# Kernel optimization log

Measured on AMD Instinct MI355X. Metric: run time of the kernel, lower is better.

Reference implementation:

```python
import jax, jax.numpy as jnp
import numpy as np

B_, L, DM = 2, 1024, 1024
D_STATE, D_CONV, EXPAND = 16, 4, 2
DI = EXPAND * DM          # 2048 inner dim
DTR = DM // 16            # 64 dt rank


def setup_inputs() -> dict:
    key = jax.random.key(0)
    ks = jax.random.split(key, 16)
    g = lambda k, shp, s: jax.random.normal(k, shp, jnp.float32) * s
    inp = {
        "x": g(ks[0], (B_, L, DM), 1.0),
        "ln_g": jnp.ones((DM,), jnp.float32),
        "ln_b": jnp.zeros((DM,), jnp.float32),
        "in_proj_w": g(ks[1], (2 * DI, DM), (2.0 / (DM + 2 * DI)) ** 0.5),
        "conv_w": g(ks[2], (DI, 1, D_CONV), (2.0 / D_CONV) ** 0.5),
        "conv_b": jnp.zeros((DI,), jnp.float32),
        "dtin_w": g(ks[3], (DTR, DI), (2.0 / (DI + DTR)) ** 0.5),
        "dtin_b": jnp.zeros((DTR,), jnp.float32),
        "dt_w": g(ks[4], (DI, DTR), DTR ** -0.5),
        "dt_b": jnp.log(jnp.expm1(jax.random.uniform(ks[5], (DI,), jnp.float32, 1e-3, 0.1))),  # inverse-softplus of dt in [dt_min, dt_max]
        "B_w": g(ks[6], (D_STATE, DI), DI ** -0.5),
        "C_w": g(ks[7], (D_STATE, DI), DI ** -0.5),
        "A_log": jnp.log(jnp.broadcast_to(jnp.arange(1, D_STATE + 1, dtype=jnp.float32), (DI, D_STATE))),
        "D": jnp.ones((DI,), jnp.float32),
        "out_w": g(ks[8], (DM, DI), (2.0 / (DM + DI)) ** 0.5),
    }
    return inp


def _layernorm(x, g, b, eps=1e-5):
    mu = jnp.mean(x, -1, keepdims=True)
    var = jnp.mean(jnp.square(x - mu), -1, keepdims=True)
    return (x - mu) * jax.lax.rsqrt(var + eps) * g + b


def _selective_scan(u, dt, Bm, Cm, A, Dp):
    # u,dt: (b,l,di); Bm,Cm: (b,l,n); A: (di,n)
    def step(h, inp):
        dt_t, B_t, C_t, u_t = inp  # (b,di),(b,n),(b,n),(b,di)
        dA = jnp.exp(dt_t[..., None] * A)                       # (b,di,n)
        h = h * dA + (dt_t * u_t)[..., None] * B_t[:, None, :]   # (b,di,n)
        y = jnp.einsum("bdn,bn->bd", h, C_t)
        return h, y

    tm = lambda a: jnp.swapaxes(a, 0, 1)  # time-major
    h0 = jnp.zeros((u.shape[0], u.shape[2], A.shape[1]), u.dtype)
    _, ys = jax.lax.scan(step, h0, (tm(dt), tm(Bm), tm(Cm), tm(u)))
    return jnp.swapaxes(ys, 0, 1) + u * Dp  # (b,l,di)


def reference(x, ln_g, ln_b, in_proj_w, conv_w, conv_b, dtin_w, dtin_b,
              dt_w, dt_b, B_w, C_w, A_log, D, out_w):
    residual = x
    xn = _layernorm(x, ln_g, ln_b)
    xz = xn @ in_proj_w.T                       # (b,l,2*di)
    x_proj, z = jnp.split(xz, 2, axis=-1)
    # causal depthwise conv1d (left pad d_conv-1, truncate to seq_len)
    xp = jnp.pad(x_proj, ((0, 0), (D_CONV - 1, 0), (0, 0)))
    x_conv = conv_b
    for k in range(D_CONV):
        x_conv = x_conv + conv_w[:, 0, k] * xp[:, k:k + L, :]
    x_conv = jax.nn.silu(x_conv)
    dt_in = x_conv @ dtin_w.T + dtin_b          # (b,l,dtr)
    dt = jax.nn.softplus(dt_in @ dt_w.T + dt_b) # (b,l,di)
    Bm = x_conv @ B_w.T                         # (b,l,n)
    Cm = x_conv @ C_w.T
    A = -jnp.exp(A_log)                         # (di,n)
    y = _selective_scan(x_conv, dt, Bm, Cm, A, D)
    y = y * jax.nn.silu(z)
    return y @ out_w.T + residual
```

## Files before the change

### kernel.cpp

```cpp
#include <hip/hip_runtime.h>
#include <hip/hip_bf16.h>
#include <cstdint>

#define BL    2
#define LSEQ  1024
#define DMOD  1024
#define DIN   2048
#define NST   16
#define DTRK  64
#define MR    (BL*LSEQ)

#define CCH 32
#define TCH 32
#define KSPLIT 8

typedef __bf16 bf16x8 __attribute__((ext_vector_type(8)));
typedef float  f32x4  __attribute__((ext_vector_type(4)));

#if __has_builtin(__builtin_amdgcn_exp2f)
#define EXP2F(x) __builtin_amdgcn_exp2f(x)
#else
#define EXP2F(x) exp2f(x)
#endif
#define LOG2E 1.4426950408889634f

__device__ __forceinline__ void glds16(const void* g, const void* l) {
    __builtin_amdgcn_global_load_lds(
        (__attribute__((address_space(1))) void*)(uintptr_t)(g),
        (__attribute__((address_space(3))) void*)(uint32_t)(uintptr_t)(l),
        16, 0, 0);
}

template <int MODE, int TM, int TN, int BK>
__global__ __launch_bounds__(256, 3) void gemm_bt(
    const __hip_bfloat16* __restrict__ A, int lda,
    const __hip_bfloat16* __restrict__ Bw, int ldb,
    int M, int N, int Ksl,
    void* __restrict__ e0, void* __restrict__ e1,
    const float* __restrict__ bias)
{
    constexpr int WM = TM / 2, WN = TN / 2;
    constexpr int MT = WM / 16, NT = WN / 16;
    constexpr int C8 = BK / 8;
    constexpr int RPP = 256 / C8;
    constexpr int PA = TM / RPP, PB = TN / RPP;
    __shared__ __align__(16) __hip_bfloat16 sA[2][TM * BK];
    __shared__ __align__(16) __hip_bfloat16 sB[2][TN * BK];

    auto SW = [](int row) { return (BK == 32) ? ((row >> 1) & 3) : (row & 7); };

    int bx = blockIdx.x, by = blockIdx.y;
    if ((gridDim.y & 7) == 0) {
        const int bid = blockIdx.x + gridDim.x * blockIdx.y;
        const int xcd = bid & 7, s = bid >> 3;
        bx = s % gridDim.x;
        by = (s / gridDim.x) * 8 + xcd;
    }
    const int m0 = by * TM;
    const int n0 = bx * TN;
    const int k0 = blockIdx.z * Ksl;
    const int tid = threadIdx.x;
    const int w = tid >> 6, lane = tid & 63;
    const int wm = (w >> 1) * WM, wn = (w & 1) * WN;
    const int lrow = lane & 15, lq = lane >> 4;

    const int r0 = tid / C8;
    const int q = ((tid % C8) - SW(r0)) & (C8 - 1);
    const __hip_bfloat16* pa[PA];
    const __hip_bfloat16* pb[PB];
#pragma unroll
    for (int p = 0; p < PA; p++) pa[p] = A + (size_t)(m0 + r0 + RPP * p) * lda + k0 + q * 8;
#pragma unroll
    for (int p = 0; p < PB; p++) pb[p] = Bw + (size_t)(n0 + r0 + RPP * p) * ldb + k0 + q * 8;

    f32x4 acc[MT][NT];
#pragma unroll
    for (int i = 0; i < MT; i++)
#pragma unroll
        for (int j = 0; j < NT; j++) { acc[i][j][0]=0.f; acc[i][j][1]=0.f; acc[i][j][2]=0.f; acc[i][j][3]=0.f; }

    const int nk = Ksl / BK;
#pragma unroll
    for (int p = 0; p < PA; p++) glds16(pa[p], &sA[0][(tid + 256 * p) * 8]);
#pragma unroll
    for (int p = 0; p < PB; p++) glds16(pb[p], &sB[0][(tid + 256 * p) * 8]);

    for (int kb = 0; kb < nk; ++kb) {
        const int cur = kb & 1, nxt = cur ^ 1;
        __syncthreads();
        if (kb + 1 < nk) {
#pragma unroll
            for (int p = 0; p < PA; p++) { pa[p] += BK; glds16(pa[p], &sA[nxt][(tid + 256 * p) * 8]); }
#pragma unroll
            for (int p = 0; p < PB; p++) { pb[p] += BK; glds16(pb[p], &sB[nxt][(tid + 256 * p) * 8]); }
        }
#pragma unroll
        for (int s = 0; s < BK / 32; s++) {
            bf16x8 af[MT], bb[NT];
#pragma unroll
            for (int mt = 0; mt < MT; mt++) {
                const int row = wm + mt * 16 + lrow;
                const int pc = ((s * 4 + lq) + SW(row)) & (C8 - 1);
                af[mt] = *(const bf16x8*)&sA[cur][row * BK + pc * 8];
            }
#pragma unroll
            for (int nt = 0; nt < NT; nt++) {
                const int row = wn + nt * 16 + lrow;
                const int pc = ((s * 4 + lq) + SW(row)) & (C8 - 1);
                bb[nt] = *(const bf16x8*)&sB[cur][row * BK + pc * 8];
            }
#pragma unroll
            for (int mt = 0; mt < MT; mt++)
#pragma unroll
                for (int nt = 0; nt < NT; nt++)
                    acc[mt][nt] = __builtin_amdgcn_mfma_f32_16x16x32_bf16(af[mt], bb[nt], acc[mt][nt], 0, 0, 0);
        }
    }

#pragma unroll
    for (int mt = 0; mt < MT; mt++) {
#pragma unroll
        for (int nt = 0; nt < NT; nt++) {
            const int gn = n0 + wn + nt * 16 + lrow;
            if (gn >= N) continue;
            const int gmb = m0 + wm + mt * 16 + lq * 4;
#pragma unroll
            for (int r = 0; r < 4; r++) {
                const int gm = gmb + r;
                const float v = acc[mt][nt][r];
                if (MODE == 0) {
                    if (gn < DIN) ((__hip_bfloat16*)e0)[(size_t)gm * DIN + gn] = __float2bfloat16(v);
                    else {
                        const float s = v / (1.f + __expf(-v));
                        ((__hip_bfloat16*)e1)[(size_t)gm * DIN + (gn - DIN)] = __float2bfloat16(s);
                    }
                } else if (MODE == 1) {
                    ((float*)e0)[((size_t)blockIdx.z * M + gm) * 96 + gn] = v;
                } else if (MODE == 2) {
                    const float xx = v + bias[gn];
                    const float sp = (xx > 20.f) ? xx : log1pf(__expf(xx));
                    ((__hip_bfloat16*)e0)[(size_t)gm * N + gn] = __float2bfloat16(sp);
                } else {
                    atomicAdd((float*)e0 + (size_t)gm * N + gn, v);
                }
            }
        }
    }
}

__global__ void ep1_kernel(const float* __restrict__ part, const float* __restrict__ dtin_b,
                           __hip_bfloat16* __restrict__ dtinb, float* __restrict__ Bmf,
                           float* __restrict__ Cmf) {
    const int i = blockIdx.x * 256 + threadIdx.x;
    if (i >= MR * 96) return;
    const int m = i / 96, n = i - m * 96;
    float s = 0.f;
#pragma unroll
    for (int z = 0; z < KSPLIT; z++) s += part[((size_t)z * MR + m) * 96 + n];
    if (n < 64)      dtinb[(size_t)m * 64 + n] = __float2bfloat16(s + dtin_b[n]);
    else if (n < 80) Bmf[(size_t)m * NST + (n - 64)] = s;
    else             Cmf[(size_t)m * NST + (n - 80)] = s;
}

#define NCVT 1654784
#define NCPY 524288
__global__ void prep_kernel(const float* __restrict__ x, const float* __restrict__ ln_g,
                            const float* __restrict__ ln_b,
                            const float* __restrict__ w_in, const float* __restrict__ dtin_w,
                            const float* __restrict__ B_w, const float* __restrict__ C_w,
                            const float* __restrict__ dt_w, const float* __restrict__ out_w,
                            __hip_bfloat16* __restrict__ w1b, __hip_bfloat16* __restrict__ wpb,
                            __hip_bfloat16* __restrict__ dtwb, __hip_bfloat16* __restrict__ owb,
                            __hip_bfloat16* __restrict__ xn, float* __restrict__ out)
{
    const int b = blockIdx.x;
    const int tid = threadIdx.x;
    if (b < MR) {
        const float4 v = ((const float4*)(x + (size_t)b * DMOD))[tid];
        float s  = v.x + v.y + v.z + v.w;
        float sq = v.x * v.x + v.y * v.y + v.z * v.z + v.w * v.w;
#pragma unroll
        for (int off = 32; off >= 1; off >>= 1) {
            s  += __shfl_down(s, off, 64);
            sq += __shfl_down(sq, off, 64);
        }
        __shared__ float red[8];
        const int w = tid >> 6, lane = tid & 63;
        if (lane == 0) { red[w] = s; red[4 + w] = sq; }
        __syncthreads();
        s  = red[0] + red[1] + red[2] + red[3];
        sq = red[4] + red[5] + red[6] + red[7];
        const float mean = s * (1.f / DMOD);
        const float rstd = rsqrtf(sq * (1.f / DMOD) - mean * mean + 1e-5f);
        const int col = tid * 4;
        const float vv[4] = {v.x, v.y, v.z, v.w};
#pragma unroll
        for (int i = 0; i < 4; i++)
            xn[(size_t)b * DMOD + col + i] =
                __float2bfloat16((vv[i] - mean) * rstd * ln_g[col + i] + ln_b[col + i]);
        return;
    }
    const int nb = gridDim.x - MR;
    for (int v4 = (b - MR) * 256 + tid; v4 < NCVT + NCPY; v4 += nb * 256) {
        if (v4 >= NCVT) {
            ((float4*)out)[v4 - NCVT] = ((const float4*)x)[v4 - NCVT];
            continue;
        }
        const int i = v4 * 4;
        const float* s; __hip_bfloat16* dk;
        if      (i < 4194304) { s = w_in   + i;             dk = w1b  + i; }
        else if (i < 4325376) { s = dtin_w + (i - 4194304); dk = wpb  + (i - 4194304); }
        else if (i < 4358144) { s = B_w    + (i - 4325376); dk = wpb  + 131072 + (i - 4325376); }
        else if (i < 4390912) { s = C_w    + (i - 4358144); dk = wpb  + 163840 + (i - 4358144); }
        else if (i < 4521984) { s = dt_w   + (i - 4390912); dk = dtwb + (i - 4390912); }
        else                  { s = out_w  + (i - 4521984); dk = owb  + (i - 4521984); }
        const float4 f = *(const float4*)s;
        ushort4 o;
        o.x = (unsigned short)(__hip_bfloat16_raw(__float2bfloat16(f.x)).x);
        o.y = (unsigned short)(__hip_bfloat16_raw(__float2bfloat16(f.y)).x);
        o.z = (unsigned short)(__hip_bfloat16_raw(__float2bfloat16(f.z)).x);
        o.w = (unsigned short)(__hip_bfloat16_raw(__float2bfloat16(f.w)).x);
        *(ushort4*)dk = o;
    }
}

__global__ void conv_silu_kernel(const __hip_bfloat16* __restrict__ xp, const float* __restrict__ cw,
                                 const float* __restrict__ cb,
                                 __hip_bfloat16* __restrict__ xcb) {
    const int d = blockIdx.x * 256 + threadIdx.x;
    const int m0 = blockIdx.y * 32;
    const int l0 = m0 & (LSEQ - 1);
    const float w0 = cw[d * 4], w1 = cw[d * 4 + 1], w2 = cw[d * 4 + 2], w3 = cw[d * 4 + 3];
    const float cbd = cb[d];
    float x0 = 0.f, x1 = 0.f, x2 = 0.f;
    if (l0 != 0) {
        x0 = __bfloat162float(xp[(size_t)(m0 - 3) * DIN + d]);
        x1 = __bfloat162float(xp[(size_t)(m0 - 2) * DIN + d]);
        x2 = __bfloat162float(xp[(size_t)(m0 - 1) * DIN + d]);
    }
#pragma unroll 4
    for (int i = 0; i < 32; i++) {
        const float x3 = __bfloat162float(xp[(size_t)(m0 + i) * DIN + d]);
        const float a = cbd + w0 * x0 + w1 * x1 + w2 * x2 + w3 * x3;
        const float sv = a / (1.f + __expf(-a));
        xcb[(size_t)(m0 + i) * DIN + d] = __float2bfloat16(sv);
        x0 = x1; x1 = x2; x2 = x3;
    }
}


__global__ __launch_bounds__(256) void scan_p1(
    const __hip_bfloat16* __restrict__ dt, const __hip_bfloat16* __restrict__ u,
    const float* __restrict__ Bm, const float* __restrict__ A_log,
    float* __restrict__ Aprod, float* __restrict__ Bacc)
{
    __shared__ float sB[TCH * NST];
    const int blk = blockIdx.x;
    const int bb = blk >> 9, c = (blk >> 4) & 31, dtile = blk & 15;
    const int tid = threadIdx.x;
    const int nh = tid & 1, dl = tid >> 1;
    const int d = dtile * 128 + dl;
    const int row0 = bb * LSEQ + c * TCH;

    sB[tid]       = Bm[(size_t)row0 * NST + tid];
    sB[tid + 256] = Bm[(size_t)row0 * NST + tid + 256];
    __syncthreads();

    float a2[8];
    {
        const float4 al0 = *(const float4*)&A_log[(size_t)d * NST + nh * 8];
        const float4 al1 = *(const float4*)&A_log[(size_t)d * NST + nh * 8 + 4];
        a2[0] = -__expf(al0.x) * LOG2E; a2[1] = -__expf(al0.y) * LOG2E;
        a2[2] = -__expf(al0.z) * LOG2E; a2[3] = -__expf(al0.w) * LOG2E;
        a2[4] = -__expf(al1.x) * LOG2E; a2[5] = -__expf(al1.y) * LOG2E;
        a2[6] = -__expf(al1.z) * LOG2E; a2[7] = -__expf(al1.w) * LOG2E;
    }
    const __hip_bfloat16* pdt = dt + (size_t)row0 * DIN + d;
    const __hip_bfloat16* pu  = u  + (size_t)row0 * DIN + d;
    float h[8], Ap[8];
#pragma unroll
    for (int j = 0; j < 8; j++) { h[j] = 0.f; Ap[j] = 1.f; }

#pragma unroll 4
    for (int t = 0; t < TCH; t++) {
        const float dtv = __bfloat162float(pdt[t * DIN]);
        const float uv  = __bfloat162float(pu[t * DIN]);
        const float du = dtv * uv;
        float bv[8];
        *(float4*)&bv[0] = *(const float4*)&sB[t * NST + nh * 8];
        *(float4*)&bv[4] = *(const float4*)&sB[t * NST + nh * 8 + 4];
#pragma unroll
        for (int j = 0; j < 8; j++) {
            const float e = EXP2F(dtv * a2[j]);
            Ap[j] *= e;
            h[j] = h[j] * e + du * bv[j];
        }
    }
    const size_t idx = (((size_t)bb * CCH + c) * DIN + d) * NST + nh * 8;
    *(float4*)&Aprod[idx]     = make_float4(Ap[0], Ap[1], Ap[2], Ap[3]);
    *(float4*)&Aprod[idx + 4] = make_float4(Ap[4], Ap[5], Ap[6], Ap[7]);
    *(float4*)&Bacc[idx]      = make_float4(h[0], h[1], h[2], h[3]);
    *(float4*)&Bacc[idx + 4]  = make_float4(h[4], h[5], h[6], h[7]);
}

__global__ __launch_bounds__(256) void scan_p2(
    const float* __restrict__ Aprod, const float* __restrict__ Bacc,
    float* __restrict__ hstart)
{
    const int i = blockIdx.x * 256 + threadIdx.x;
    const int bb = i >> 15;
    const int dn = i & 32767;
    float hs = 0.f;
#pragma unroll
    for (int c = 0; c < CCH; c++) {
        const size_t idx = (((size_t)bb * CCH + c) << 15) + dn;
        hstart[idx] = hs;
        hs = Aprod[idx] * hs + Bacc[idx];
    }
}

__global__ __launch_bounds__(256) void scan_p3(
    const __hip_bfloat16* __restrict__ dt, const __hip_bfloat16* __restrict__ u,
    const float* __restrict__ Bm, const float* __restrict__ Cm,
    const float* __restrict__ A_log, const float* __restrict__ Dp,
    const __hip_bfloat16* __restrict__ zs, const float* __restrict__ hstart,
    __hip_bfloat16* __restrict__ y)
{
    __shared__ float sB[TCH * NST], sC[TCH * NST];
    const int blk = blockIdx.x;
    const int bb = blk >> 9, c = (blk >> 4) & 31, dtile = blk & 15;
    const int tid = threadIdx.x;
    const int nh = tid & 1, dl = tid >> 1;
    const int d = dtile * 128 + dl;
    const int row0 = bb * LSEQ + c * TCH;

    sB[tid]       = Bm[(size_t)row0 * NST + tid];
    sB[tid + 256] = Bm[(size_t)row0 * NST + tid + 256];
    sC[tid]       = Cm[(size_t)row0 * NST + tid];
    sC[tid + 256] = Cm[(size_t)row0 * NST + tid + 256];
    __syncthreads();

    float a2[8];
    {
        const float4 al0 = *(const float4*)&A_log[(size_t)d * NST + nh * 8];
        const float4 al1 = *(const float4*)&A_log[(size_t)d * NST + nh * 8 + 4];
        a2[0] = -__expf(al0.x) * LOG2E; a2[1] = -__expf(al0.y) * LOG2E;
        a2[2] = -__expf(al0.z) * LOG2E; a2[3] = -__expf(al0.w) * LOG2E;
        a2[4] = -__expf(al1.x) * LOG2E; a2[5] = -__expf(al1.y) * LOG2E;
        a2[6] = -__expf(al1.z) * LOG2E; a2[7] = -__expf(al1.w) * LOG2E;
    }
    const float Dd = Dp[d];
    const size_t idx = (((size_t)bb * CCH + c) * DIN + d) * NST + nh * 8;
    float h[8];
    *(float4*)&h[0] = *(const float4*)&hstart[idx];
    *(float4*)&h[4] = *(const float4*)&hstart[idx + 4];

    const __hip_bfloat16* pdt = dt + (size_t)row0 * DIN + d;
    const __hip_bfloat16* pu  = u  + (size_t)row0 * DIN + d;
    const __hip_bfloat16* pz  = zs + (size_t)row0 * DIN + d;
    __hip_bfloat16* py = y + (size_t)row0 * DIN + d;

#pragma unroll 2
    for (int t = 0; t < TCH; t++) {
        const float dtv = __bfloat162float(pdt[t * DIN]);
        const float uv  = __bfloat162float(pu[t * DIN]);
        const float du = dtv * uv;
        float bv[8], cv[8];
        *(float4*)&bv[0] = *(const float4*)&sB[t * NST + nh * 8];
        *(float4*)&bv[4] = *(const float4*)&sB[t * NST + nh * 8 + 4];
        *(float4*)&cv[0] = *(const float4*)&sC[t * NST + nh * 8];
        *(float4*)&cv[4] = *(const float4*)&sC[t * NST + nh * 8 + 4];
        float yp = 0.f;
#pragma unroll
        for (int j = 0; j < 8; j++) {
            const float e = EXP2F(dtv * a2[j]);
            h[j] = h[j] * e + du * bv[j];
            yp += h[j] * cv[j];
        }
        yp += __shfl_xor(yp, 1, 64);
        if (nh == 0) {
            const float zv = __bfloat162float(pz[t * DIN]);
            py[t * DIN] = __float2bfloat16((yp + uv * Dd) * zv);
        }
    }
}

extern "C" void kernel_launch(void* const* d_in, const int* in_sizes, int n_in,
                              void* d_out, int out_size, void* d_ws, size_t ws_size,
                              hipStream_t stream) {
    const float* x      = (const float*)d_in[0];
    const float* ln_g   = (const float*)d_in[1];
    const float* ln_b   = (const float*)d_in[2];
    const float* w_in   = (const float*)d_in[3];
    const float* conv_w = (const float*)d_in[4];
    const float* conv_b = (const float*)d_in[5];
    const float* dtin_w = (const float*)d_in[6];
    const float* dtin_b = (const float*)d_in[7];
    const float* dt_w   = (const float*)d_in[8];
    const float* dt_b   = (const float*)d_in[9];
    const float* B_w    = (const float*)d_in[10];
    const float* C_w    = (const float*)d_in[11];
    const float* A_log  = (const float*)d_in[12];
    const float* Dp     = (const float*)d_in[13];
    const float* out_w  = (const float*)d_in[14];
    float* out = (float*)d_out;

    char* ws = (char*)d_ws;
    auto alloc = [&](size_t bytes) { char* p = ws; ws += (bytes + 255) & ~255ull; return p; };
    __hip_bfloat16* w1b   = (__hip_bfloat16*)alloc((size_t)4096 * 1024 * 2);
    __hip_bfloat16* wpb   = (__hip_bfloat16*)alloc((size_t)96 * 2048 * 2);
    __hip_bfloat16* dtwb  = (__hip_bfloat16*)alloc((size_t)2048 * 64 * 2);
    __hip_bfloat16* owb   = (__hip_bfloat16*)alloc((size_t)1024 * 2048 * 2);
    __hip_bfloat16* xnb   = (__hip_bfloat16*)alloc((size_t)MR * DMOD * 2);
    __hip_bfloat16* xprojb= (__hip_bfloat16*)alloc((size_t)MR * DIN * 2);
    __hip_bfloat16* zs    = (__hip_bfloat16*)alloc((size_t)MR * DIN * 2);
    __hip_bfloat16* xcb   = (__hip_bfloat16*)alloc((size_t)MR * DIN * 2);
    __hip_bfloat16* dtinb = (__hip_bfloat16*)alloc((size_t)MR * 64 * 2);
    float*          Bmf   = (float*)alloc((size_t)MR * NST * 4);
    float*          Cmf   = (float*)alloc((size_t)MR * NST * 4);
    __hip_bfloat16* dtb   = (__hip_bfloat16*)alloc((size_t)MR * DIN * 2);
    __hip_bfloat16* yb    = (__hip_bfloat16*)alloc((size_t)MR * DIN * 2);
    float*          Aprod = (float*)alloc((size_t)BL * CCH * DIN * NST * 4);
    float*          Bacc  = (float*)alloc((size_t)BL * CCH * DIN * NST * 4);
    float*          hstart= (float*)alloc((size_t)BL * CCH * DIN * NST * 4);
    float*          part  = (float*)w1b;

    prep_kernel<<<MR + 896, 256, 0, stream>>>(x, ln_g, ln_b, w_in, dtin_w, B_w, C_w, dt_w,
                                              out_w, w1b, wpb, dtwb, owb, xnb, out);

    gemm_bt<0, 128, 128, 32><<<dim3(32, 16, 1), 256, 0, stream>>>(
        xnb, 1024, w1b, 1024, MR, 4096, 1024, xprojb, zs, nullptr);

    conv_silu_kernel<<<dim3(8, 64), 256, 0, stream>>>(xprojb, conv_w, conv_b, xcb);

    gemm_bt<1, 64, 128, 64><<<dim3(1, 32, KSPLIT), 256, 0, stream>>>(
        xcb, 2048, wpb, 2048, MR, 96, 2048 / KSPLIT, part, nullptr, nullptr);
    ep1_kernel<<<(MR * 96 + 255) / 256, 256, 0, stream>>>(part, dtin_b, dtinb, Bmf, Cmf);

    gemm_bt<2, 64, 128, 64><<<dim3(16, 32, 1), 256, 0, stream>>>(
        dtinb, 64, dtwb, 64, MR, DIN, 64, dtb, nullptr, dt_b);

    scan_p1<<<BL * CCH * 16, 256, 0, stream>>>(dtb, xcb, Bmf, A_log, Aprod, Bacc);
    scan_p2<<<BL * DIN * NST / 256, 256, 0, stream>>>(Aprod, Bacc, hstart);
    scan_p3<<<BL * CCH * 16, 256, 0, stream>>>(dtb, xcb, Bmf, Cmf, A_log, Dp, zs, hstart, yb);

    gemm_bt<3, 128, 128, 32><<<dim3(8, 16, 2), 256, 0, stream>>>(
        yb, 2048, owb, 2048, MR, DMOD, 1024, out, nullptr, nullptr);
}
```

Baseline: 244.2 us.

## Fuse causal conv+SiLU into in_proj GEMM epilogue and drop split-K atomics in out_proj

New measurement: 233.5 us. -4.4%, faster.

```diff
diff --git a/kernel.cpp b/kernel.cpp
--- a/kernel.cpp
+++ b/kernel.cpp
@@ -37,8 +37,10 @@
     const __hip_bfloat16* __restrict__ Bw, int ldb,
     int M, int N, int Ksl,
     void* __restrict__ e0, void* __restrict__ e1,
-    const float* __restrict__ bias)
+    const float* __restrict__ bias, const float* __restrict__ bias2)
 {
+    constexpr bool FUSE = (MODE == 0);
+    static_assert(!FUSE || BK == 64, "fused conv epilogue assumes BK=64");
     constexpr int WM = TM / 2, WN = TN / 2;
     constexpr int MT = WM / 16, NT = WN / 16;
     constexpr int C8 = BK / 8;
@@ -46,6 +48,7 @@
     constexpr int PA = TM / RPP, PB = TN / RPP;
     __shared__ __align__(16) __hip_bfloat16 sA[2][TM * BK];
     __shared__ __align__(16) __hip_bfloat16 sB[2][TN * BK];
+    __shared__ __align__(16) __hip_bfloat16 sH[2][(FUSE ? 16 : 1) * 64];
 
     auto SW = [](int row) { return (BK == 32) ? ((row >> 1) & 3) : (row & 7); };
 
@@ -73,17 +76,30 @@
 #pragma unroll
     for (int p = 0; p < PB; p++) pb[p] = Bw + (size_t)(n0 + r0 + RPP * p) * ldb + k0 + q * 8;
 
+    const bool isX = FUSE && (n0 < DIN);
+    const __hip_bfloat16* ph = nullptr;
+    if (FUSE) {
+        const int rh = tid >> 3;
+        const int qh = ((tid & 7) - (rh & 7)) & 7;
+        ph = A + (size_t)(m0 - 16 + rh) * lda + k0 + qh * 8;
+    }
+
     f32x4 acc[MT][NT];
 #pragma unroll
     for (int i = 0; i < MT; i++)
 #pragma unroll
         for (int j = 0; j < NT; j++) { acc[i][j][0]=0.f; acc[i][j][1]=0.f; acc[i][j][2]=0.f; acc[i][j][3]=0.f; }
+    f32x4 hacc[FUSE ? NT : 1];
+    if (FUSE)
+#pragma unroll
+        for (int j = 0; j < NT; j++) { hacc[j][0]=0.f; hacc[j][1]=0.f; hacc[j][2]=0.f; hacc[j][3]=0.f; }
 
     const int nk = Ksl / BK;
 #pragma unroll
     for (int p = 0; p < PA; p++) glds16(pa[p], &sA[0][(tid + 256 * p) * 8]);
 #pragma unroll
     for (int p = 0; p < PB; p++) glds16(pb[p], &sB[0][(tid + 256 * p) * 8]);
+    if (isX && tid < 128) glds16(ph, &sH[0][tid * 8]);
 
     for (int kb = 0; kb < nk; ++kb) {
         const int cur = kb & 1, nxt = cur ^ 1;
@@ -93,6 +109,7 @@
             for (int p = 0; p < PA; p++) { pa[p] += BK; glds16(pa[p], &sA[nxt][(tid + 256 * p) * 8]); }
 #pragma unroll
             for (int p = 0; p < PB; p++) { pb[p] += BK; glds16(pb[p], &sB[nxt][(tid + 256 * p) * 8]); }
+            if (isX && tid < 128) { ph += BK; glds16(ph, &sH[nxt][tid * 8]); }
         }
 #pragma unroll
         for (int s = 0; s < BK / 32; s++) {
@@ -114,9 +131,79 @@
 #pragma unroll
                 for (int nt = 0; nt < NT; nt++)
                     acc[mt][nt] = __builtin_amdgcn_mfma_f32_16x16x32_bf16(af[mt], bb[nt], acc[mt][nt], 0, 0, 0);
-        }
-    }
-
+            if (isX && w < 2) {
+                const int pcH = ((s * 4 + lq) + (lrow & 7)) & 7;
+                const bf16x8 afh = *(const bf16x8*)&sH[cur][lrow * 64 + pcH * 8];
+#pragma unroll
+                for (int nt = 0; nt < NT; nt++)
+                    hacc[nt] = __builtin_amdgcn_mfma_f32_16x16x32_bf16(afh, bb[nt], hacc[nt], 0, 0, 0);
+            }
+        }
+    }
+
+    if (MODE == 0 && isX) {
+        __syncthreads();
+        __hip_bfloat16* tile = (__hip_bfloat16*)&sB[0][0];
+        constexpr int TS = TN + 8;
+#pragma unroll
+        for (int mt = 0; mt < MT; mt++)
+#pragma unroll
+            for (int nt = 0; nt < NT; nt++) {
+                const int col = wn + nt * 16 + lrow;
+#pragma unroll
+                for (int r = 0; r < 4; r++)
+                    tile[(16 + wm + mt * 16 + lq * 4 + r) * TS + col] = __float2bfloat16(acc[mt][nt][r]);
+            }
+        if (w < 2) {
+#pragma unroll
+            for (int nt = 0; nt < NT; nt++) {
+                const int col = wn + nt * 16 + lrow;
+#pragma unroll
+                for (int r = 0; r < 4; r++)
+                    tile[(lq * 4 + r) * TS + col] = __float2bfloat16(hacc[nt][r]);
+            }
+        }
+        __syncthreads();
+        const int c2 = (tid & 63) * 2;
+        const int rg = tid >> 6;
+        const int dg = n0 + c2;
+        const float4 wA = *(const float4*)&bias[dg * 4];
+        const float4 wB = *(const float4*)&bias[dg * 4 + 4];
+        const float cbA = bias2[dg], cbB = bias2[dg + 1];
+        const int l0 = m0 & (LSEQ - 1);
+        const int rbase = rg * 16;
+        float a0, a1, a2, b0, b1, b2;
+        if (l0 == 0 && rg == 0) {
+            a0 = a1 = a2 = b0 = b1 = b2 = 0.f;
+        } else {
+            const int hr = 16 + rbase - 3;
+            a0 = __bfloat162float(tile[(hr + 0) * TS + c2]);
+            b0 = __bfloat162float(tile[(hr + 0) * TS + c2 + 1]);
+            a1 = __bfloat162float(tile[(hr + 1) * TS + c2]);
+            b1 = __bfloat162float(tile[(hr + 1) * TS + c2 + 1]);
+            a2 = __bfloat162float(tile[(hr + 2) * TS + c2]);
+            b2 = __bfloat162float(tile[(hr + 2) * TS + c2 + 1]);
+        }
+        __hip_bfloat16* xcbp = (__hip_bfloat16*)e0;
+#pragma unroll 4
+        for (int i = 0; i < 16; i++) {
+            const int row = rbase + i;
+            const float a3 = __bfloat162float(tile[(16 + row) * TS + c2]);
+            const float b3 = __bfloat162float(tile[(16 + row) * TS + c2 + 1]);
+            float sa = cbA + wA.x * a0 + wA.y * a1 + wA.z * a2 + wA.w * a3;
+            float sb = cbB + wB.x * b0 + wB.y * b1 + wB.z * b2 + wB.w * b3;
+            sa = sa / (1.f + __expf(-sa));
+            sb = sb / (1.f + __expf(-sb));
+            __hip_bfloat16 ha = __float2bfloat16(sa), hb = __float2bfloat16(sb);
+            ushort2 o;
+            o.x = (unsigned short)__hip_bfloat16_raw(ha).x;
+            o.y = (unsigned short)__hip_bfloat16_raw(hb).x;
+            *(ushort2*)&xcbp[(size_t)(m0 + row) * DIN + dg] = o;
+            a0 = a1; a1 = a2; a2 = a3;
+            b0 = b1; b1 = b2; b2 = b3;
+        }
+        return;
+    }
 #pragma unroll
     for (int mt = 0; mt < MT; mt++) {
 #pragma unroll
@@ -129,11 +216,8 @@
                 const int gm = gmb + r;
                 const float v = acc[mt][nt][r];
                 if (MODE == 0) {
-                    if (gn < DIN) ((__hip_bfloat16*)e0)[(size_t)gm * DIN + gn] = __float2bfloat16(v);
-                    else {
-                        const float s = v / (1.f + __expf(-v));
-                        ((__hip_bfloat16*)e1)[(size_t)gm * DIN + (gn - DIN)] = __float2bfloat16(s);
-                    }
+                    const float s = v / (1.f + __expf(-v));
+                    ((__hip_bfloat16*)e1)[(size_t)gm * DIN + (gn - DIN)] = __float2bfloat16(s);
                 } else if (MODE == 1) {
                     ((float*)e0)[((size_t)blockIdx.z * M + gm) * 96 + gn] = v;
                 } else if (MODE == 2) {
@@ -141,7 +225,7 @@
                     const float sp = (xx > 20.f) ? xx : log1pf(__expf(xx));
                     ((__hip_bfloat16*)e0)[(size_t)gm * N + gn] = __float2bfloat16(sp);
                 } else {
-                    atomicAdd((float*)e0 + (size_t)gm * N + gn, v);
+                    ((float*)e0)[(size_t)gm * N + gn] = v + ((const float*)e1)[(size_t)gm * N + gn];
                 }
             }
         }
@@ -163,7 +247,6 @@
 }
 
 #define NCVT 1654784
-#define NCPY 524288
 __global__ void prep_kernel(const float* __restrict__ x, const float* __restrict__ ln_g,
                             const float* __restrict__ ln_b,
                             const float* __restrict__ w_in, const float* __restrict__ dtin_w,
@@ -171,7 +254,7 @@
                             const float* __restrict__ dt_w, const float* __restrict__ out_w,
                             __hip_bfloat16* __restrict__ w1b, __hip_bfloat16* __restrict__ wpb,
                             __hip_bfloat16* __restrict__ dtwb, __hip_bfloat16* __restrict__ owb,
-                            __hip_bfloat16* __restrict__ xn, float* __restrict__ out)
+                            __hip_bfloat16* __restrict__ xn)
 {
     const int b = blockIdx.x;
     const int tid = threadIdx.x;
@@ -201,11 +284,7 @@
         return;
     }
     const int nb = gridDim.x - MR;
-    for (int v4 = (b - MR) * 256 + tid; v4 < NCVT + NCPY; v4 += nb * 256) {
-        if (v4 >= NCVT) {
-            ((float4*)out)[v4 - NCVT] = ((const float4*)x)[v4 - NCVT];
-            continue;
-        }
+    for (int v4 = (b - MR) * 256 + tid; v4 < NCVT; v4 += nb * 256) {
         const int i = v4 * 4;
         const float* s; __hip_bfloat16* dk;
         if      (i < 4194304) { s = w_in   + i;             dk = w1b  + i; }
@@ -221,30 +300,6 @@
         o.z = (unsigned short)(__hip_bfloat16_raw(__float2bfloat16(f.z)).x);
         o.w = (unsigned short)(__hip_bfloat16_raw(__float2bfloat16(f.w)).x);
         *(ushort4*)dk = o;
-    }
-}
-
-__global__ void conv_silu_kernel(const __hip_bfloat16* __restrict__ xp, const float* __restrict__ cw,
-                                 const float* __restrict__ cb,
-                                 __hip_bfloat16* __restrict__ xcb) {
-    const int d = blockIdx.x * 256 + threadIdx.x;
-    const int m0 = blockIdx.y * 32;
-    const int l0 = m0 & (LSEQ - 1);
-    const float w0 = cw[d * 4], w1 = cw[d * 4 + 1], w2 = cw[d * 4 + 2], w3 = cw[d * 4 + 3];
-    const float cbd = cb[d];
-    float x0 = 0.f, x1 = 0.f, x2 = 0.f;
-    if (l0 != 0) {
-        x0 = __bfloat162float(xp[(size_t)(m0 - 3) * DIN + d]);
-        x1 = __bfloat162float(xp[(size_t)(m0 - 2) * DIN + d]);
-        x2 = __bfloat162float(xp[(size_t)(m0 - 1) * DIN + d]);
-    }
-#pragma unroll 4
-    for (int i = 0; i < 32; i++) {
-        const float x3 = __bfloat162float(xp[(size_t)(m0 + i) * DIN + d]);
-        const float a = cbd + w0 * x0 + w1 * x1 + w2 * x2 + w3 * x3;
-        const float sv = a / (1.f + __expf(-a));
-        xcb[(size_t)(m0 + i) * DIN + d] = __float2bfloat16(sv);
-        x0 = x1; x1 = x2; x2 = x3;
     }
 }
 
@@ -412,7 +467,6 @@
     __hip_bfloat16* dtwb  = (__hip_bfloat16*)alloc((size_t)2048 * 64 * 2);
     __hip_bfloat16* owb   = (__hip_bfloat16*)alloc((size_t)1024 * 2048 * 2);
     __hip_bfloat16* xnb   = (__hip_bfloat16*)alloc((size_t)MR * DMOD * 2);
-    __hip_bfloat16* xprojb= (__hip_bfloat16*)alloc((size_t)MR * DIN * 2);
     __hip_bfloat16* zs    = (__hip_bfloat16*)alloc((size_t)MR * DIN * 2);
     __hip_bfloat16* xcb   = (__hip_bfloat16*)alloc((size_t)MR * DIN * 2);
     __hip_bfloat16* dtinb = (__hip_bfloat16*)alloc((size_t)MR * 64 * 2);
@@ -426,24 +480,22 @@
     float*          part  = (float*)w1b;
 
     prep_kernel<<<MR + 896, 256, 0, stream>>>(x, ln_g, ln_b, w_in, dtin_w, B_w, C_w, dt_w,
-                                              out_w, w1b, wpb, dtwb, owb, xnb, out);
-
-    gemm_bt<0, 128, 128, 32><<<dim3(32, 16, 1), 256, 0, stream>>>(
-        xnb, 1024, w1b, 1024, MR, 4096, 1024, xprojb, zs, nullptr);
-
-    conv_silu_kernel<<<dim3(8, 64), 256, 0, stream>>>(xprojb, conv_w, conv_b, xcb);
+                                              out_w, w1b, wpb, dtwb, owb, xnb);
+
+    gemm_bt<0, 64, 128, 64><<<dim3(32, 32, 1), 256, 0, stream>>>(
+        xnb, 1024, w1b, 1024, MR, 4096, 1024, xcb, zs, conv_w, conv_b);
 
     gemm_bt<1, 64, 128, 64><<<dim3(1, 32, KSPLIT), 256, 0, stream>>>(
-        xcb, 2048, wpb, 2048, MR, 96, 2048 / KSPLIT, part, nullptr, nullptr);
+        xcb, 2048, wpb, 2048, MR, 96, 2048 / KSPLIT, part, nullptr, nullptr, nullptr);
     ep1_kernel<<<(MR * 96 + 255) / 256, 256, 0, stream>>>(part, dtin_b, dtinb, Bmf, Cmf);
 
     gemm_bt<2, 64, 128, 64><<<dim3(16, 32, 1), 256, 0, stream>>>(
-        dtinb, 64, dtwb, 64, MR, DIN, 64, dtb, nullptr, dt_b);
+        dtinb, 64, dtwb, 64, MR, DIN, 64, dtb, nullptr, dt_b, nullptr);
 
     scan_p1<<<BL * CCH * 16, 256, 0, stream>>>(dtb, xcb, Bmf, A_log, Aprod, Bacc);
     scan_p2<<<BL * DIN * NST / 256, 256, 0, stream>>>(Aprod, Bacc, hstart);
     scan_p3<<<BL * CCH * 16, 256, 0, stream>>>(dtb, xcb, Bmf, Cmf, A_log, Dp, zs, hstart, yb);
 
-    gemm_bt<3, 128, 128, 32><<<dim3(8, 16, 2), 256, 0, stream>>>(
-        yb, 2048, owb, 2048, MR, DMOD, 1024, out, nullptr, nullptr);
-}
+    gemm_bt<3, 64, 64, 64><<<dim3(16, 32, 1), 256, 0, stream>>>(
+        yb, 2048, owb, 2048, MR, DMOD, 2048, out, (void*)x, nullptr, nullptr);
+}
```
